# Kernel optimization log

Hardware: AMD Instinct MI355X
Metric: run time of the kernel (lower is better)

## Reference

```python
import jax, jax.numpy as jnp
import numpy as np

N_NODES = 100000
N_EDGES = 3200000
D = 128
B = 4


def gcn_conv(x, row, col, W, b, n):
    # PyG GCNConv: x' = D^{-1/2}(A+I)D^{-1/2} (x W) + b
    xw = x @ W  # [N, out]
    ones = jnp.ones((row.shape[0],), dtype=x.dtype)
    deg = jax.ops.segment_sum(ones, col, num_segments=n) + 1.0  # self-loop
    dinv = jax.lax.rsqrt(deg)  # deg > 0 because of self-loops
    norm = dinv[row] * dinv[col]  # [E]
    msg = xw[row] * norm[:, None]  # gather + scale
    agg = jax.ops.segment_sum(msg, col, num_segments=n)  # scatter-add
    agg = agg + (dinv * dinv)[:, None] * xw  # self-loop contribution
    return agg + b


def setup_inputs() -> dict:
    key = jax.random.key(0)
    ks = jax.random.split(key, 10)
    x = jax.random.normal(ks[0], (N_NODES, D), dtype=jnp.float32)
    edge_index = jax.random.randint(ks[1], (2, N_EDGES), 0, N_NODES, dtype=jnp.int64)
    question_embeddings = jax.random.normal(ks[2], (B, D), dtype=jnp.float32)
    s = 1.0 / np.sqrt(D)
    W1 = jax.random.uniform(ks[3], (D, D), jnp.float32, -s, s)
    b1 = jnp.zeros((D,), jnp.float32)
    W2 = jax.random.uniform(ks[4], (D, D), jnp.float32, -s, s)
    b2 = jnp.zeros((D,), jnp.float32)
    Wq = jax.random.uniform(ks[5], (D, D), jnp.float32, -s, s)
    bq = jax.random.uniform(ks[6], (D,), jnp.float32, -s, s)
    return {"x": x, "edge_index": edge_index, "question_embeddings": question_embeddings,
            "W1": W1, "b1": b1, "W2": W2, "b2": b2, "Wq": Wq, "bq": bq}


def reference(x, edge_index, question_embeddings, W1, b1, W2, b2, Wq, bq):
    n = x.shape[0]
    row, col = edge_index[0], edge_index[1]
    h = jax.nn.relu(gcn_conv(x, row, col, W1, b1, n))  # [N, H]
    h = gcn_conv(h, row, col, W2, b2, n)  # [N, H]
    q = question_embeddings @ Wq + bq  # [B, H]
    out = h[None, :, :] + q[:, None, :]  # [B, N, H]
    return jax.nn.log_softmax(out, axis=1)  # softmax over node dim (torch dim=1)
```

## Files before the change

### kernel.cpp

```cpp
#include <hip/hip_runtime.h>
#include <math.h>

#define DD 128
#define CT 16384

typedef unsigned int uint;
typedef unsigned short u16;

typedef __attribute__((ext_vector_type(8))) __bf16 bf16x8;
typedef __attribute__((ext_vector_type(4))) float f32x4;
typedef __attribute__((ext_vector_type(4))) uint uint4v;
typedef __attribute__((ext_vector_type(8))) u16 u16x8;


__device__ inline uint bf16bits(float a) {
  uint u = __float_as_uint(a);
  return (u + 0x7fffu + ((u >> 16) & 1u)) >> 16;
}

__device__ inline uint pack_bf16x2(float a, float b) {
  return bf16bits(a) | (bf16bits(b) << 16);
}


__global__ __launch_bounds__(256) void k_hist(const int* __restrict__ col,
                                              int* __restrict__ bucketCnt,
                                              int E, int NB) {
  __shared__ int hist[512];
  int tid = threadIdx.x;
  long e0 = (long)blockIdx.x * CT;
  int cnt = (int)min((long)CT, (long)E - e0);
  for (int i = tid; i < NB; i += 256) hist[i] = 0;
  __syncthreads();
  for (int i = tid; i < cnt; i += 256) atomicAdd(&hist[col[e0 + i] >> 8], 1);
  __syncthreads();
  for (int i = tid; i < NB; i += 256)
    if (hist[i]) atomicAdd(&bucketCnt[i], hist[i]);
}

__global__ __launch_bounds__(1024) void k_scan_block(const int* __restrict__ bucketCnt,
                                                     int* __restrict__ bucketBase,
                                                     int* __restrict__ gcursor, int NB) {
  __shared__ int s[1024];
  int t = threadIdx.x;
  int v = (t < NB) ? bucketCnt[t] : 0;
  s[t] = v;
  __syncthreads();
  for (int o = 1; o < 1024; o <<= 1) {
    int add = (t >= o) ? s[t - o] : 0;
    __syncthreads();
    s[t] += add;
    __syncthreads();
  }
  if (t < NB) {
    int e = s[t] - v;
    bucketBase[t] = e;
    gcursor[t] = e;
  }
  if (t == NB - 1) bucketBase[NB] = s[t];
}

__global__ __launch_bounds__(256) void k_coarse(const int* __restrict__ row,
                                                const int* __restrict__ col,
                                                int* __restrict__ gcursor,
                                                uint* __restrict__ coarse,
                                                int E, int NB) {
  __shared__ int hist[512];
  __shared__ int base[512];
  int tid = threadIdx.x;
  long e0 = (long)blockIdx.x * CT;
  int cnt = (int)min((long)CT, (long)E - e0);
  for (int i = tid; i < NB; i += 256) hist[i] = 0;
  __syncthreads();
  for (int i = tid; i < cnt; i += 256) atomicAdd(&hist[col[e0 + i] >> 8], 1);
  __syncthreads();
  for (int i = tid; i < NB; i += 256) {
    base[i] = atomicAdd(&gcursor[i], hist[i]);
    hist[i] = 0;
  }
  __syncthreads();
  for (int i = tid; i < cnt; i += 256) {
    int c = col[e0 + i];
    int r = row[e0 + i];
    int b = c >> 8;
    int p = base[b] + atomicAdd(&hist[b], 1);
    coarse[p] = ((uint)r << 8) | (uint)(c & 255);
  }
}

__global__ __launch_bounds__(256) void k_finalize(const uint* __restrict__ coarse,
                                                  const int* __restrict__ bucketBase,
                                                  int* __restrict__ off,
                                                  float* __restrict__ dinv,
                                                  int* __restrict__ srt, int n, int NB) {
  __shared__ int hist[256];
  __shared__ int s[256];
  __shared__ int cur[256];
  int tid = threadIdx.x;
  int b = blockIdx.x;
  int base = bucketBase[b], endb = bucketBase[b + 1];
  int cnt = endb - base;
  int node0 = b << 8;
  hist[tid] = 0;
  __syncthreads();
  for (int i = tid; i < cnt; i += 256) atomicAdd(&hist[coarse[base + i] & 255u], 1);
  __syncthreads();
  int deg = hist[tid];
  s[tid] = deg;
  __syncthreads();
  for (int o = 1; o < 256; o <<= 1) {
    int add = (tid >= o) ? s[tid - o] : 0;
    __syncthreads();
    s[tid] += add;
    __syncthreads();
  }
  int excl = base + s[tid] - deg;
  int node = node0 + tid;
  if (node < n) {
    off[node] = excl;
    dinv[node] = rsqrtf(1.0f + (float)deg);
  }
  if (node == n - 1) off[n] = endb;
  cur[tid] = excl;
  __syncthreads();
  for (int i = tid; i < cnt; i += 256) {
    uint e = coarse[base + i];
    int pos = atomicAdd(&cur[e & 255u], 1);
    srt[pos] = (int)(e >> 8);
  }
}


__global__ __launch_bounds__(256) void k_prepw(const float* __restrict__ W1,
                                               const float* __restrict__ W2,
                                               u16* __restrict__ o1h, u16* __restrict__ o1l,
                                               u16* __restrict__ o2h, u16* __restrict__ o2l) {
  const float* W = blockIdx.x ? W2 : W1;
  u16* oh = blockIdx.x ? o2h : o1h;
  u16* ol = blockIdx.x ? o2l : o1l;
  for (int i = threadIdx.x; i < 16384; i += 256) {
    int k = i >> 7, c = i & 127;
    float v = W[i];
    uint hb = bf16bits(v);
    float hv = __uint_as_float(hb << 16);
    uint lb = bf16bits(v - hv);
    uint uidx = (((uint)c << 6) + ((uint)k >> 1)) ^ (((uint)c & 7u) << 2);
    int p = (int)((uidx << 1) | ((uint)k & 1u));
    oh[p] = (u16)hb;
    ol[p] = (u16)lb;
  }
}


__global__ __launch_bounds__(256, 2) void k_gemm(const float* __restrict__ X,
                                                 const u16* __restrict__ gWh,
                                                 const u16* __restrict__ gWl,
                                                 const float* __restrict__ dinv,
                                                 uint* __restrict__ msg, int n) {
  __shared__ uint Wh[8192];
  __shared__ uint Wl[8192];
  int tid = threadIdx.x;
  for (int i = tid; i < 2048; i += 256) ((uint4*)Wh)[i] = ((const uint4*)gWh)[i];
  for (int i = tid; i < 2048; i += 256) ((uint4*)Wl)[i] = ((const uint4*)gWl)[i];

  int lane = tid & 63, wv = tid >> 6;
  int s_ = lane & 15, g = lane >> 4;
  int row0 = blockIdx.x * 128 + wv * 32;

  f32x4 acc[2][8];
#pragma unroll
  for (int a = 0; a < 2; a++)
#pragma unroll
    for (int b = 0; b < 8; b++) acc[a][b] = (f32x4)0.f;

  __syncthreads();

#pragma unroll
  for (int kc = 0; kc < 4; kc++) {
    uint4v ah[2], al[2];
#pragma unroll
    for (int sub = 0; sub < 2; sub++) {
      int r = row0 + sub * 16 + s_;
      float4 v0, v1;
      if (r < n) {
        const float* xp = X + (size_t)r * DD + kc * 32 + g * 8;
        v0 = ((const float4*)xp)[0];
        v1 = ((const float4*)xp)[1];
      } else {
        v0 = make_float4(0.f, 0.f, 0.f, 0.f);
        v1 = v0;
      }
      uint h0 = bf16bits(v0.x), h1 = bf16bits(v0.y), h2 = bf16bits(v0.z), h3 = bf16bits(v0.w);
      uint h4 = bf16bits(v1.x), h5 = bf16bits(v1.y), h6 = bf16bits(v1.z), h7 = bf16bits(v1.w);
      ah[sub][0] = h0 | (h1 << 16);
      ah[sub][1] = h2 | (h3 << 16);
      ah[sub][2] = h4 | (h5 << 16);
      ah[sub][3] = h6 | (h7 << 16);
      al[sub][0] = pack_bf16x2(v0.x - __uint_as_float(h0 << 16), v0.y - __uint_as_float(h1 << 16));
      al[sub][1] = pack_bf16x2(v0.z - __uint_as_float(h2 << 16), v0.w - __uint_as_float(h3 << 16));
      al[sub][2] = pack_bf16x2(v1.x - __uint_as_float(h4 << 16), v1.y - __uint_as_float(h5 << 16));
      al[sub][3] = pack_bf16x2(v1.z - __uint_as_float(h6 << 16), v1.w - __uint_as_float(h7 << 16));
    }
    int koff2 = (kc * 32 + g * 8) >> 1;
#pragma unroll
    for (int ct = 0; ct < 8; ct++) {
      int c = ct * 16 + s_;
      int uo = (int)(((uint)(c << 6) + (uint)koff2) ^ (((uint)c & 7u) << 2));
      bf16x8 bh = __builtin_bit_cast(bf16x8, *(const u16x8*)&Wh[uo]);
      bf16x8 bl = __builtin_bit_cast(bf16x8, *(const u16x8*)&Wl[uo]);
#pragma unroll
      for (int sub = 0; sub < 2; sub++) {
        bf16x8 av = __builtin_bit_cast(bf16x8, ah[sub]);
        bf16x8 lv = __builtin_bit_cast(bf16x8, al[sub]);
        acc[sub][ct] = __builtin_amdgcn_mfma_f32_16x16x32_bf16(av, bh, acc[sub][ct], 0, 0, 0);
        acc[sub][ct] = __builtin_amdgcn_mfma_f32_16x16x32_bf16(lv, bh, acc[sub][ct], 0, 0, 0);
        acc[sub][ct] = __builtin_amdgcn_mfma_f32_16x16x32_bf16(av, bl, acc[sub][ct], 0, 0, 0);
      }
    }
  }

#pragma unroll
  for (int sub = 0; sub < 2; sub++) {
#pragma unroll
    for (int q = 0; q < 4; q++) {
      int rq = row0 + sub * 16 + g * 4 + q;
      if (rq < n) {
        float di = dinv[rq];
        uint* mrow = msg + (size_t)rq * 64;
#pragma unroll
        for (int ct = 0; ct < 4; ct++) {
          uint u = pack_bf16x2(acc[sub][ct][q] * di, acc[sub][ct + 4][q] * di);
          mrow[ct * 16 + s_] = u;
        }
      }
    }
  }
}


__global__ __launch_bounds__(256) void k_agg(const uint* __restrict__ msg,
                                             const int* __restrict__ srt,
                                             const int* __restrict__ off,
                                             const float* __restrict__ dinv,
                                             const float* __restrict__ bias,
                                             float* __restrict__ out, int n, int relu) {
  int lane = threadIdx.x & 63;
  int s_ = lane & 15, g = lane >> 4;
  int node = blockIdx.x * 4 + (threadIdx.x >> 6);
  if (node >= n) return;
  int beg = off[node], end = off[node + 1];
  float a0 = 0.f, a1 = 0.f, a2 = 0.f, a3 = 0.f, a4 = 0.f, a5 = 0.f, a6 = 0.f, a7 = 0.f;
  const uint4* m4 = (const uint4*)msg;
  for (int t = beg; t < end; t += 64) {
    int nt = end - t;
    if (nt > 64) nt = 64;
    int idx = srt[t + (lane < nt ? lane : nt - 1)];
    for (int k = 0; k < nt; k += 16) {
      uint4 r[4];
      if (k + 16 <= nt) {
#pragma unroll
        for (int u = 0; u < 4; u++) {
          int src = __shfl(idx, k + u * 4 + g);
          r[u] = m4[(size_t)src * 16 + s_];
        }
      } else {
#pragma unroll
        for (int u = 0; u < 4; u++) {
          int e = k + u * 4 + g;
          int src = __shfl(idx, e < nt ? e : nt - 1);
          r[u] = m4[(size_t)src * 16 + s_];
          if (e >= nt) r[u] = make_uint4(0u, 0u, 0u, 0u);
        }
      }
#pragma unroll
      for (int u = 0; u < 4; u++) {
        a0 += __uint_as_float(r[u].x << 16); a4 += __uint_as_float(r[u].x & 0xffff0000u);
        a1 += __uint_as_float(r[u].y << 16); a5 += __uint_as_float(r[u].y & 0xffff0000u);
        a2 += __uint_as_float(r[u].z << 16); a6 += __uint_as_float(r[u].z & 0xffff0000u);
        a3 += __uint_as_float(r[u].w << 16); a7 += __uint_as_float(r[u].w & 0xffff0000u);
      }
    }
  }
#define RED(x) x += __shfl_xor(x, 16); x += __shfl_xor(x, 32);
  RED(a0) RED(a1) RED(a2) RED(a3) RED(a4) RED(a5) RED(a6) RED(a7)
#undef RED
  uint4 rs = m4[(size_t)node * 16 + s_];
  a0 += __uint_as_float(rs.x << 16); a4 += __uint_as_float(rs.x & 0xffff0000u);
  a1 += __uint_as_float(rs.y << 16); a5 += __uint_as_float(rs.y & 0xffff0000u);
  a2 += __uint_as_float(rs.z << 16); a6 += __uint_as_float(rs.z & 0xffff0000u);
  a3 += __uint_as_float(rs.w << 16); a7 += __uint_as_float(rs.w & 0xffff0000u);
  float di = dinv[node];
  if (g == 0) {
    float4 bv = ((const float4*)bias)[s_];
    float4 o = make_float4(di * a0 + bv.x, di * a1 + bv.y, di * a2 + bv.z, di * a3 + bv.w);
    if (relu) {
      o.x = fmaxf(o.x, 0.f); o.y = fmaxf(o.y, 0.f); o.z = fmaxf(o.z, 0.f); o.w = fmaxf(o.w, 0.f);
    }
    ((float4*)(out + (size_t)node * DD))[s_] = o;
  } else if (g == 1) {
    float4 bv = ((const float4*)(bias + 64))[s_];
    float4 o = make_float4(di * a4 + bv.x, di * a5 + bv.y, di * a6 + bv.z, di * a7 + bv.w);
    if (relu) {
      o.x = fmaxf(o.x, 0.f); o.y = fmaxf(o.y, 0.f); o.z = fmaxf(o.z, 0.f); o.w = fmaxf(o.w, 0.f);
    }
    ((float4*)(out + (size_t)node * DD + 64))[s_] = o;
  }
}


__global__ __launch_bounds__(256) void k_colstat(const float* __restrict__ h, int n,
                                                 float* __restrict__ PM,
                                                 float* __restrict__ PS) {
  __shared__ float sm[128], ss[128];
  int d = threadIdx.x & 127, sub = threadIdx.x >> 7;
  float m = -3.4e38f, s = 0.f;
  for (int r = blockIdx.x * 2 + sub; r < n; r += gridDim.x * 2) {
    float v = h[(size_t)r * DD + d];
    float nm = fmaxf(m, v);
    s = s * __expf(m - nm) + __expf(v - nm);
    m = nm;
  }
  if (sub) { sm[d] = m; ss[d] = s; }
  __syncthreads();
  if (!sub) {
    float m2 = sm[d], s2 = ss[d];
    float nm = fmaxf(m, m2);
    float so = s * __expf(m - nm) + s2 * __expf(m2 - nm);
    PM[blockIdx.x * 128 + d] = nm;
    PS[blockIdx.x * 128 + d] = so;
  }
}

__global__ __launch_bounds__(64) void k_lsemerge(const float* __restrict__ PM,
                                                 const float* __restrict__ PS,
                                                 float* __restrict__ L, int nb) {
  int d = blockIdx.x;
  int lane = threadIdx.x;
  float m = -3.4e38f, s = 0.f;
  for (int p = lane; p < nb; p += 64) {
    float m2 = PM[p * 128 + d], s2 = PS[p * 128 + d];
    float nm = fmaxf(m, m2);
    s = s * __expf(m - nm) + s2 * __expf(m2 - nm);
    m = nm;
  }
#pragma unroll
  for (int o = 1; o < 64; o <<= 1) {
    float m2 = __shfl_xor(m, o), s2 = __shfl_xor(s, o);
    float nm = fmaxf(m, m2);
    s = s * __expf(m - nm) + s2 * __expf(m2 - nm);
    m = nm;
  }
  if (lane == 0) L[d] = m + logf(s);
}


__global__ __launch_bounds__(256) void k_final(const float* __restrict__ h,
                                               const float* __restrict__ L,
                                               float* __restrict__ out, int n, int B) {
  int idx = blockIdx.x * 256 + threadIdx.x;
  int nd4 = n * 32;
  if (idx >= nd4) return;
  int c4 = idx & 31;
  float4 hv = ((const float4*)h)[idx];
  float4 lv = ((const float4*)L)[c4];
  float4 r = make_float4(hv.x - lv.x, hv.y - lv.y, hv.z - lv.z, hv.w - lv.w);
  float4* o = (float4*)out;
  for (int b = 0; b < B; b++) o[(size_t)idx + (size_t)b * nd4] = r;
}


extern "C" void kernel_launch(void* const* d_in, const int* in_sizes, int n_in,
                              void* d_out, int out_size, void* d_ws, size_t ws_size,
                              hipStream_t stream) {
  const float* x  = (const float*)d_in[0];
  const int*   ei = (const int*)d_in[1];
  const float* W1 = (const float*)d_in[3];
  const float* b1 = (const float*)d_in[4];
  const float* W2 = (const float*)d_in[5];
  const float* b2 = (const float*)d_in[6];

  int n = in_sizes[0] / DD;
  int E = in_sizes[1] / 2;
  int B = out_size / (n * DD);
  const int* row = ei;
  const int* col = ei + E;

  float* out = (float*)d_out;
  size_t nd = (size_t)n * DD;
  float* bufA = out;
  float* bufB = out + nd;
  int* srt = (int*)(out + 2 * nd);
  uint* coarse = (uint*)((char*)srt + (size_t)4 * E);
  uint* msg = (uint*)coarse;
  char* sm = (char*)(out + 3 * nd);
  auto alloc = [&](size_t bytes) -> char* {
    char* p = sm;
    sm += (bytes + 63) & ~(size_t)63;
    return p;
  };
  float* dinv = (float*)alloc(sizeof(float) * n);
  int* off = (int*)alloc(sizeof(int) * (n + 1));
  int NB = (n + 255) / 256;
  int* bucketCnt = (int*)alloc(sizeof(int) * NB);
  int* bucketBase = (int*)alloc(sizeof(int) * (NB + 1));
  int* gcursor = (int*)alloc(sizeof(int) * NB);
  u16* wt1h = (u16*)alloc(32768);
  u16* wt1l = (u16*)alloc(32768);
  u16* wt2h = (u16*)alloc(32768);
  u16* wt2l = (u16*)alloc(32768);
  float* PM = (float*)alloc(sizeof(float) * 512 * 128);
  float* PS = (float*)alloc(sizeof(float) * 512 * 128);
  float* L = (float*)d_ws;

  int gC = (E + CT - 1) / CT;

  hipMemsetAsync(bucketCnt, 0, sizeof(int) * NB, stream);
  k_prepw<<<2, 256, 0, stream>>>(W1, W2, wt1h, wt1l, wt2h, wt2l);
  k_hist<<<gC, 256, 0, stream>>>(col, bucketCnt, E, NB);
  k_scan_block<<<1, 1024, 0, stream>>>(bucketCnt, bucketBase, gcursor, NB);
  k_coarse<<<gC, 256, 0, stream>>>(row, col, gcursor, coarse, E, NB);
  k_finalize<<<NB, 256, 0, stream>>>(coarse, bucketBase, off, dinv, srt, n, NB);

  int gG = (n + 127) / 128;
  k_gemm<<<gG, 256, 0, stream>>>(x, wt1h, wt1l, dinv, msg, n);
  k_agg<<<(n + 3) / 4, 256, 0, stream>>>(msg, srt, off, dinv, b1, bufA, n, 1);
  k_gemm<<<gG, 256, 0, stream>>>(bufA, wt2h, wt2l, dinv, msg, n);
  k_agg<<<(n + 3) / 4, 256, 0, stream>>>(msg, srt, off, dinv, b2, bufB, n, 0);

  k_colstat<<<512, 256, 0, stream>>>(bufB, n, PM, PS);
  k_lsemerge<<<128, 64, 0, stream>>>(PM, PS, L, 512);
  k_final<<<(n * 32 + 255) / 256, 256, 0, stream>>>(bufB, L, out, n, B);
}
```

Before: 727.5 us.

## Store messages in 8 feature panels and aggregate per panel for cache locality

The GEMM epilogue now writes the bf16 message matrix as 8 column panels, each [n][32 bytes], instead of row-major 256-byte rows. The aggregation kernel launches 8 blocks per chunk of 16 nodes, one per panel, so each panel's working set (about 3.2 MB) can stay resident in L2/MALL during the random gathers. The cost is that each edge index is now read 8 times, and each gather moves only 32 bytes, so memory transactions are smaller and per-edge overhead goes up.

```diff
diff --git a/kernel.cpp b/kernel.cpp
--- a/kernel.cpp
+++ b/kernel.cpp
@@ -226,11 +226,11 @@
       int rq = row0 + sub * 16 + g * 4 + q;
       if (rq < n) {
         float di = dinv[rq];
-        uint* mrow = msg + (size_t)rq * 64;
 #pragma unroll
         for (int ct = 0; ct < 4; ct++) {
           uint u = pack_bf16x2(acc[sub][ct][q] * di, acc[sub][ct + 4][q] * di);
-          mrow[ct * 16 + s_] = u;
+          int m = ct * 16 + s_;
+          msg[((size_t)(m >> 3) * n + rq) * 8 + (m & 7)] = u;
         }
       }
     }
@@ -244,66 +244,58 @@
                                              const float* __restrict__ dinv,
                                              const float* __restrict__ bias,
                                              float* __restrict__ out, int n, int relu) {
-  int lane = threadIdx.x & 63;
-  int s_ = lane & 15, g = lane >> 4;
-  int node = blockIdx.x * 4 + (threadIdx.x >> 6);
-  if (node >= n) return;
-  int beg = off[node], end = off[node + 1];
+  int lane = threadIdx.x & 63, wv = threadIdx.x >> 6;
+  int panel = blockIdx.x & 7, chunk = blockIdx.x >> 3;
+  int sub = lane & 15;
+  int el = sub >> 1, half = sub & 1;
+  int node = chunk * 16 + wv * 4 + (lane >> 4);
+  const uint4* mp = (const uint4*)msg + (size_t)panel * n * 2;
+  int beg = 0, end = 0;
+  if (node < n) { beg = off[node]; end = off[node + 1]; }
   float a0 = 0.f, a1 = 0.f, a2 = 0.f, a3 = 0.f, a4 = 0.f, a5 = 0.f, a6 = 0.f, a7 = 0.f;
-  const uint4* m4 = (const uint4*)msg;
-  for (int t = beg; t < end; t += 64) {
+  for (int t = beg; t < end; t += 16) {
     int nt = end - t;
-    if (nt > 64) nt = 64;
-    int idx = srt[t + (lane < nt ? lane : nt - 1)];
-    for (int k = 0; k < nt; k += 16) {
-      uint4 r[4];
-      if (k + 16 <= nt) {
-#pragma unroll
-        for (int u = 0; u < 4; u++) {
-          int src = __shfl(idx, k + u * 4 + g);
-          r[u] = m4[(size_t)src * 16 + s_];
-        }
-      } else {
-#pragma unroll
-        for (int u = 0; u < 4; u++) {
-          int e = k + u * 4 + g;
-          int src = __shfl(idx, e < nt ? e : nt - 1);
-          r[u] = m4[(size_t)src * 16 + s_];
-          if (e >= nt) r[u] = make_uint4(0u, 0u, 0u, 0u);
-        }
-      }
-#pragma unroll
-      for (int u = 0; u < 4; u++) {
-        a0 += __uint_as_float(r[u].x << 16); a4 += __uint_as_float(r[u].x & 0xffff0000u);
-        a1 += __uint_as_float(r[u].y << 16); a5 += __uint_as_float(r[u].y & 0xffff0000u);
-        a2 += __uint_as_float(r[u].z << 16); a6 += __uint_as_float(r[u].z & 0xffff0000u);
-        a3 += __uint_as_float(r[u].w << 16); a7 += __uint_as_float(r[u].w & 0xffff0000u);
+    if (nt > 16) nt = 16;
+    int idx = srt[t + (sub < nt ? sub : nt - 1)];
+    for (int k = 0; k < nt; k += 8) {
+      int e = k + el;
+      int src = __shfl(idx, (lane & 48) + (e < nt ? e : nt - 1));
+      if (e < nt) {
+        uint4 r = mp[(size_t)src * 2 + half];
+        a0 += __uint_as_float(r.x << 16); a1 += __uint_as_float(r.x & 0xffff0000u);
+        a2 += __uint_as_float(r.y << 16); a3 += __uint_as_float(r.y & 0xffff0000u);
+        a4 += __uint_as_float(r.z << 16); a5 += __uint_as_float(r.z & 0xffff0000u);
+        a6 += __uint_as_float(r.w << 16); a7 += __uint_as_float(r.w & 0xffff0000u);
       }
     }
   }
-#define RED(x) x += __shfl_xor(x, 16); x += __shfl_xor(x, 32);
-  RED(a0) RED(a1) RED(a2) RED(a3) RED(a4) RED(a5) RED(a6) RED(a7)
-#undef RED
-  uint4 rs = m4[(size_t)node * 16 + s_];
-  a0 += __uint_as_float(rs.x << 16); a4 += __uint_as_float(rs.x & 0xffff0000u);
-  a1 += __uint_as_float(rs.y << 16); a5 += __uint_as_float(rs.y & 0xffff0000u);
-  a2 += __uint_as_float(rs.z << 16); a6 += __uint_as_float(rs.z & 0xffff0000u);
-  a3 += __uint_as_float(rs.w << 16); a7 += __uint_as_float(rs.w & 0xffff0000u);
-  float di = dinv[node];
-  if (g == 0) {
-    float4 bv = ((const float4*)bias)[s_];
-    float4 o = make_float4(di * a0 + bv.x, di * a1 + bv.y, di * a2 + bv.z, di * a3 + bv.w);
+#pragma unroll
+  for (int o = 2; o <= 8; o <<= 1) {
+    a0 += __shfl_xor(a0, o); a1 += __shfl_xor(a1, o);
+    a2 += __shfl_xor(a2, o); a3 += __shfl_xor(a3, o);
+    a4 += __shfl_xor(a4, o); a5 += __shfl_xor(a5, o);
+    a6 += __shfl_xor(a6, o); a7 += __shfl_xor(a7, o);
+  }
+  if (node < n && el == 0) {
+    uint4 rs = mp[(size_t)node * 2 + half];
+    a0 += __uint_as_float(rs.x << 16); a1 += __uint_as_float(rs.x & 0xffff0000u);
+    a2 += __uint_as_float(rs.y << 16); a3 += __uint_as_float(rs.y & 0xffff0000u);
+    a4 += __uint_as_float(rs.z << 16); a5 += __uint_as_float(rs.z & 0xffff0000u);
+    a6 += __uint_as_float(rs.w << 16); a7 += __uint_as_float(rs.w & 0xffff0000u);
+    float di = dinv[node];
+    int dlo = panel * 8 + half * 4;
+    float4 bl = *(const float4*)(bias + dlo);
+    float4 bh = *(const float4*)(bias + 64 + dlo);
+    float4 olo = make_float4(di * a0 + bl.x, di * a2 + bl.y, di * a4 + bl.z, di * a6 + bl.w);
+    float4 ohi = make_float4(di * a1 + bh.x, di * a3 + bh.y, di * a5 + bh.z, di * a7 + bh.w);
     if (relu) {
-      o.x = fmaxf(o.x, 0.f); o.y = fmaxf(o.y, 0.f); o.z = fmaxf(o.z, 0.f); o.w = fmaxf(o.w, 0.f);
+      olo.x = fmaxf(olo.x, 0.f); olo.y = fmaxf(olo.y, 0.f);
+      olo.z = fmaxf(olo.z, 0.f); olo.w = fmaxf(olo.w, 0.f);
+      ohi.x = fmaxf(ohi.x, 0.f); ohi.y = fmaxf(ohi.y, 0.f);
+      ohi.z = fmaxf(ohi.z, 0.f); ohi.w = fmaxf(ohi.w, 0.f);
     }
-    ((float4*)(out + (size_t)node * DD))[s_] = o;
-  } else if (g == 1) {
-    float4 bv = ((const float4*)(bias + 64))[s_];
-    float4 o = make_float4(di * a4 + bv.x, di * a5 + bv.y, di * a6 + bv.z, di * a7 + bv.w);
-    if (relu) {
-      o.x = fmaxf(o.x, 0.f); o.y = fmaxf(o.y, 0.f); o.z = fmaxf(o.z, 0.f); o.w = fmaxf(o.w, 0.f);
-    }
-    ((float4*)(out + (size_t)node * DD + 64))[s_] = o;
+    *(float4*)(out + (size_t)node * DD + dlo) = olo;
+    *(float4*)(out + (size_t)node * DD + 64 + dlo) = ohi;
   }
 }
 
@@ -422,10 +414,11 @@
   k_finalize<<<NB, 256, 0, stream>>>(coarse, bucketBase, off, dinv, srt, n, NB);
 
   int gG = (n + 127) / 128;
+  int gA = ((n + 15) / 16) * 8;
   k_gemm<<<gG, 256, 0, stream>>>(x, wt1h, wt1l, dinv, msg, n);
-  k_agg<<<(n + 3) / 4, 256, 0, stream>>>(msg, srt, off, dinv, b1, bufA, n, 1);
+  k_agg<<<gA, 256, 0, stream>>>(msg, srt, off, dinv, b1, bufA, n, 1);
   k_gemm<<<gG, 256, 0, stream>>>(bufA, wt2h, wt2l, dinv, msg, n);
-  k_agg<<<(n + 3) / 4, 256, 0, stream>>>(msg, srt, off, dinv, b2, bufB, n, 0);
+  k_agg<<<gA, 256, 0, stream>>>(msg, srt, off, dinv, b2, bufB, n, 0);
 
   k_colstat<<<512, 256, 0, stream>>>(bufB, n, PM, PS);
   k_lsemerge<<<128, 64, 0, stream>>>(PM, PS, L, 512);
```

Result: slower. 818.7 us (+12.5%).
